# Performance work log

Measured on AMD Instinct MI355X. Metric: run time of the kernel, lower is better.

Reference implementation:

```python
import jax, jax.numpy as jnp
import numpy as np

B, D, G = 64, 1024, 64  # batch, features==units (required by the source einsum), num_groups


def setup_inputs() -> dict:
    key = jax.random.key(0)
    ks = jax.random.split(key, 8)
    return {
        "x": jax.random.normal(ks[0], (B, D), jnp.float32),
        "gid": jax.random.randint(ks[1], (B,), 0, G, dtype=jnp.int32),
        # mean-field variational parameters per group (weights flattened to D*D as in the source)
        "w_mu": jax.random.normal(ks[2], (G, D * D), jnp.float32) * 0.05,
        "w_sigma": jax.random.normal(ks[3], (G, D * D), jnp.float32) * 0.1 - 3.0,  # raw scale params
        "b_mu": jnp.zeros((G, D), jnp.float32),
        "b_sigma": jax.random.normal(ks[4], (G, D), jnp.float32) * 0.1 - 3.0,
        # reparameterization noise (explicit so forward is deterministic)
        "eps_w": jax.random.normal(ks[5], (B, D * D), jnp.float32),
        "eps_b": jax.random.normal(ks[6], (B, D), jnp.float32),
    }


def reference(x, gid, w_mu, w_sigma, b_mu, b_sigma, eps_w, eps_b):
    # Gather group-specific posterior params and sample via reparameterization.
    # scale = softplus(raw) matches the standard tfp mean-field parameterization.
    w_samp = w_mu[gid] + jax.nn.softplus(w_sigma[gid]) * eps_w  # (B, D*D)
    b_samp = b_mu[gid] + jax.nn.softplus(b_sigma[gid]) * eps_b  # (B, D)
    # Reshape((-1, units)): (B, num_features, units) = (B, D, D)
    w = w_samp.reshape(B, D, D)
    # tf.einsum('Bup,Bp->Bu', w, x): per-sample matmul (axis1 labeled u, axis2 labeled p)
    out = jnp.einsum("bup,bp->bu", w, x) + b_samp  # (B, D)
    return jax.nn.relu(out)
```

## Files before the change

kernel.cpp:

```cpp
#include <hip/hip_runtime.h>
#include <math.h>

#define BB 64
#define DD 1024
#define GG 64
#define F4 (DD / 4)
#define ROWS 2
#define WAVES_PB 4
#define U_PER_BLOCK (ROWS * WAVES_PB)
#define BLOCKS_PER_B (DD / U_PER_BLOCK)
#define NWG (BB * BLOCKS_PER_B)

typedef float fvec4 __attribute__((ext_vector_type(4)));

__device__ __forceinline__ float softplus_fast(float z) {
    const float LOG2E = 1.44269504088896340736f;
    const float LN2   = 0.69314718055994530942f;
    float t = __builtin_amdgcn_exp2f(-LOG2E * fabsf(z));
    float l = __builtin_amdgcn_logf(1.0f + t);
    return fmaxf(z, 0.0f) + LN2 * l;
}

__global__ __launch_bounds__(256) void mld_kernel(
    const float* __restrict__ x, const int* __restrict__ gid,
    const float* __restrict__ w_mu, const float* __restrict__ w_sigma,
    const float* __restrict__ b_mu, const float* __restrict__ b_sigma,
    const float* __restrict__ eps_w, const float* __restrict__ eps_b,
    float* __restrict__ out)
{
    const int lane = (int)(threadIdx.x & 63);
    const int wid  = (int)(threadIdx.x >> 6);

    const int logical = (int)blockIdx.x;
    const int b    = logical >> 7;
    const int ublk = logical & 127;
    const int u0   = ublk * U_PER_BLOCK + wid * ROWS;
    const int g    = gid[b];

    const fvec4* __restrict__ xr  = (const fvec4*)(x + (size_t)b * DD);
    const fvec4* __restrict__ wmr = (const fvec4*)(w_mu    + ((size_t)g * DD + u0) * DD);
    const fvec4* __restrict__ wsr = (const fvec4*)(w_sigma + ((size_t)g * DD + u0) * DD);
    const fvec4* __restrict__ ewr = (const fvec4*)(eps_w   + ((size_t)b * DD + u0) * DD);

    fvec4 X[4], WM0[4], WS0[4], EW0[4], WM1[4], WS1[4], EW1[4];
    #pragma unroll
    for (int k = 0; k < 4; ++k) {
        const int i = lane + 64 * k;
        X[k]   = xr[i];
        WM0[k] = wmr[i];
        WS0[k] = wsr[i];
        EW0[k] = __builtin_nontemporal_load(ewr + i);
        WM1[k] = wmr[F4 + i];
        WS1[k] = wsr[F4 + i];
        EW1[k] = __builtin_nontemporal_load(ewr + F4 + i);
    }
    asm volatile("" ::
        "v"(X[0]),   "v"(X[1]),   "v"(X[2]),   "v"(X[3]),
        "v"(WM0[0]), "v"(WM0[1]), "v"(WM0[2]), "v"(WM0[3]),
        "v"(WS0[0]), "v"(WS0[1]), "v"(WS0[2]), "v"(WS0[3]),
        "v"(EW0[0]), "v"(EW0[1]), "v"(EW0[2]), "v"(EW0[3]),
        "v"(WM1[0]), "v"(WM1[1]), "v"(WM1[2]), "v"(WM1[3]),
        "v"(WS1[0]), "v"(WS1[1]), "v"(WS1[2]), "v"(WS1[3]),
        "v"(EW1[0]), "v"(EW1[1]), "v"(EW1[2]), "v"(EW1[3]));

    float a0 = 0.f, a1 = 0.f;
    #pragma unroll
    for (int k = 0; k < 4; ++k) {
        a0 += (WM0[k].x + softplus_fast(WS0[k].x) * EW0[k].x) * X[k].x;
        a0 += (WM0[k].y + softplus_fast(WS0[k].y) * EW0[k].y) * X[k].y;
        a0 += (WM0[k].z + softplus_fast(WS0[k].z) * EW0[k].z) * X[k].z;
        a0 += (WM0[k].w + softplus_fast(WS0[k].w) * EW0[k].w) * X[k].w;
        a1 += (WM1[k].x + softplus_fast(WS1[k].x) * EW1[k].x) * X[k].x;
        a1 += (WM1[k].y + softplus_fast(WS1[k].y) * EW1[k].y) * X[k].y;
        a1 += (WM1[k].z + softplus_fast(WS1[k].z) * EW1[k].z) * X[k].z;
        a1 += (WM1[k].w + softplus_fast(WS1[k].w) * EW1[k].w) * X[k].w;
    }

    #pragma unroll
    for (int off = 32; off > 0; off >>= 1) {
        a0 += __shfl_xor(a0, off, 64);
        a1 += __shfl_xor(a1, off, 64);
    }

    if (lane < ROWS) {
        const int u = u0 + lane;
        const size_t gu = (size_t)g * DD + u;
        const size_t bu = (size_t)b * DD + u;
        const float eb = __builtin_nontemporal_load(eps_b + bu);
        const float bs = b_mu[gu] + softplus_fast(b_sigma[gu]) * eb;
        const float o = (lane == 0 ? a0 : a1) + bs;
        out[bu] = fmaxf(o, 0.0f);
    }
}

extern "C" void kernel_launch(void* const* d_in, const int* in_sizes, int n_in,
                              void* d_out, int out_size, void* d_ws, size_t ws_size,
                              hipStream_t stream) {
    const float* x       = (const float*)d_in[0];
    const int*   gid     = (const int*)d_in[1];
    const float* w_mu    = (const float*)d_in[2];
    const float* w_sigma = (const float*)d_in[3];
    const float* b_mu    = (const float*)d_in[4];
    const float* b_sigma = (const float*)d_in[5];
    const float* eps_w   = (const float*)d_in[6];
    const float* eps_b   = (const float*)d_in[7];
    float* out = (float*)d_out;

    mld_kernel<<<NWG, 256, 0, stream>>>(x, gid, w_mu, w_sigma, b_mu, b_sigma,
                                        eps_w, eps_b, out);
}
```

Before: 113.0 us.

## Group batch rows by gid so each group's weights and softplus are loaded once

Adds a small kernel that builds per-group lists of batch indices, then launches one grid over groups instead of batch rows. Each block loads w_mu and w_sigma for its group once, computes softplus once, and loops over every batch row in that group, streaming only eps_w and x per row. This removes the duplicated reads of the group weights and the repeated softplus when several rows share a group. The cost is an extra serial launch, load imbalance because row counts per group vary, and a loop that streams eps_w without the explicit register prefetch of the old code.

```diff
diff --git a/kernel.cpp b/kernel.cpp
--- a/kernel.cpp
+++ b/kernel.cpp
@@ -5,11 +5,9 @@
 #define DD 1024
 #define GG 64
 #define F4 (DD / 4)
-#define ROWS 2
-#define WAVES_PB 4
-#define U_PER_BLOCK (ROWS * WAVES_PB)
-#define BLOCKS_PER_B (DD / U_PER_BLOCK)
-#define NWG (BB * BLOCKS_PER_B)
+#define UPB 8
+#define BLOCKS_PER_G (DD / UPB)
+#define NWG (GG * BLOCKS_PER_G)
 
 typedef float fvec4 __attribute__((ext_vector_type(4)));
 
@@ -21,8 +19,20 @@
     return fmaxf(z, 0.0f) + LN2 * l;
 }
 
-__global__ __launch_bounds__(256) void mld_kernel(
-    const float* __restrict__ x, const int* __restrict__ gid,
+__global__ void build_lists(const int* __restrict__ gid,
+                            int* __restrict__ counts, int* __restrict__ lists) {
+    const int g = (int)threadIdx.x;
+    if (g < GG) {
+        int c = 0;
+        for (int b = 0; b < BB; ++b)
+            if (gid[b] == g) lists[g * BB + (c++)] = b;
+        counts[g] = c;
+    }
+}
+
+__global__ __launch_bounds__(256) void mld_group_kernel(
+    const float* __restrict__ x,
+    const int* __restrict__ counts, const int* __restrict__ lists,
     const float* __restrict__ w_mu, const float* __restrict__ w_sigma,
     const float* __restrict__ b_mu, const float* __restrict__ b_sigma,
     const float* __restrict__ eps_w, const float* __restrict__ eps_b,
@@ -30,66 +40,66 @@
 {
     const int lane = (int)(threadIdx.x & 63);
     const int wid  = (int)(threadIdx.x >> 6);
+    const int g    = (int)blockIdx.x >> 7;
+    const int ublk = (int)blockIdx.x & 127;
+    const int n    = counts[g];
+    if (n == 0) return;
+    const int u0   = ublk * UPB + wid * 2;
 
-    const int logical = (int)blockIdx.x;
-    const int b    = logical >> 7;
-    const int ublk = logical & 127;
-    const int u0   = ublk * U_PER_BLOCK + wid * ROWS;
-    const int g    = gid[b];
-
-    const fvec4* __restrict__ xr  = (const fvec4*)(x + (size_t)b * DD);
     const fvec4* __restrict__ wmr = (const fvec4*)(w_mu    + ((size_t)g * DD + u0) * DD);
     const fvec4* __restrict__ wsr = (const fvec4*)(w_sigma + ((size_t)g * DD + u0) * DD);
-    const fvec4* __restrict__ ewr = (const fvec4*)(eps_w   + ((size_t)b * DD + u0) * DD);
 
-    fvec4 X[4], WM0[4], WS0[4], EW0[4], WM1[4], WS1[4], EW1[4];
+    fvec4 WM0[4], WM1[4], SP0[4], SP1[4];
     #pragma unroll
     for (int k = 0; k < 4; ++k) {
         const int i = lane + 64 * k;
-        X[k]   = xr[i];
         WM0[k] = wmr[i];
-        WS0[k] = wsr[i];
-        EW0[k] = __builtin_nontemporal_load(ewr + i);
         WM1[k] = wmr[F4 + i];
-        WS1[k] = wsr[F4 + i];
-        EW1[k] = __builtin_nontemporal_load(ewr + F4 + i);
-    }
-    asm volatile("" ::
-        "v"(X[0]),   "v"(X[1]),   "v"(X[2]),   "v"(X[3]),
-        "v"(WM0[0]), "v"(WM0[1]), "v"(WM0[2]), "v"(WM0[3]),
-        "v"(WS0[0]), "v"(WS0[1]), "v"(WS0[2]), "v"(WS0[3]),
-        "v"(EW0[0]), "v"(EW0[1]), "v"(EW0[2]), "v"(EW0[3]),
-        "v"(WM1[0]), "v"(WM1[1]), "v"(WM1[2]), "v"(WM1[3]),
-        "v"(WS1[0]), "v"(WS1[1]), "v"(WS1[2]), "v"(WS1[3]),
-        "v"(EW1[0]), "v"(EW1[1]), "v"(EW1[2]), "v"(EW1[3]));
-
-    float a0 = 0.f, a1 = 0.f;
-    #pragma unroll
-    for (int k = 0; k < 4; ++k) {
-        a0 += (WM0[k].x + softplus_fast(WS0[k].x) * EW0[k].x) * X[k].x;
-        a0 += (WM0[k].y + softplus_fast(WS0[k].y) * EW0[k].y) * X[k].y;
-        a0 += (WM0[k].z + softplus_fast(WS0[k].z) * EW0[k].z) * X[k].z;
-        a0 += (WM0[k].w + softplus_fast(WS0[k].w) * EW0[k].w) * X[k].w;
-        a1 += (WM1[k].x + softplus_fast(WS1[k].x) * EW1[k].x) * X[k].x;
-        a1 += (WM1[k].y + softplus_fast(WS1[k].y) * EW1[k].y) * X[k].y;
-        a1 += (WM1[k].z + softplus_fast(WS1[k].z) * EW1[k].z) * X[k].z;
-        a1 += (WM1[k].w + softplus_fast(WS1[k].w) * EW1[k].w) * X[k].w;
+        fvec4 s0 = wsr[i];
+        fvec4 s1 = wsr[F4 + i];
+        SP0[k].x = softplus_fast(s0.x); SP0[k].y = softplus_fast(s0.y);
+        SP0[k].z = softplus_fast(s0.z); SP0[k].w = softplus_fast(s0.w);
+        SP1[k].x = softplus_fast(s1.x); SP1[k].y = softplus_fast(s1.y);
+        SP1[k].z = softplus_fast(s1.z); SP1[k].w = softplus_fast(s1.w);
     }
 
-    #pragma unroll
-    for (int off = 32; off > 0; off >>= 1) {
-        a0 += __shfl_xor(a0, off, 64);
-        a1 += __shfl_xor(a1, off, 64);
-    }
+    for (int s = 0; s < n; ++s) {
+        const int b = lists[g * BB + s];
+        const fvec4* __restrict__ xr  = (const fvec4*)(x     + (size_t)b * DD);
+        const fvec4* __restrict__ ewr = (const fvec4*)(eps_w + ((size_t)b * DD + u0) * DD);
 
-    if (lane < ROWS) {
-        const int u = u0 + lane;
-        const size_t gu = (size_t)g * DD + u;
-        const size_t bu = (size_t)b * DD + u;
-        const float eb = __builtin_nontemporal_load(eps_b + bu);
-        const float bs = b_mu[gu] + softplus_fast(b_sigma[gu]) * eb;
-        const float o = (lane == 0 ? a0 : a1) + bs;
-        out[bu] = fmaxf(o, 0.0f);
+        float a0 = 0.f, a1 = 0.f;
+        #pragma unroll
+        for (int k = 0; k < 4; ++k) {
+            const int i = lane + 64 * k;
+            const fvec4 xm = xr[i];
+            const fvec4 e0 = __builtin_nontemporal_load(ewr + i);
+            const fvec4 e1 = __builtin_nontemporal_load(ewr + F4 + i);
+            a0 += (WM0[k].x + SP0[k].x * e0.x) * xm.x;
+            a0 += (WM0[k].y + SP0[k].y * e0.y) * xm.y;
+            a0 += (WM0[k].z + SP0[k].z * e0.z) * xm.z;
+            a0 += (WM0[k].w + SP0[k].w * e0.w) * xm.w;
+            a1 += (WM1[k].x + SP1[k].x * e1.x) * xm.x;
+            a1 += (WM1[k].y + SP1[k].y * e1.y) * xm.y;
+            a1 += (WM1[k].z + SP1[k].z * e1.z) * xm.z;
+            a1 += (WM1[k].w + SP1[k].w * e1.w) * xm.w;
+        }
+
+        #pragma unroll
+        for (int off = 32; off > 0; off >>= 1) {
+            a0 += __shfl_xor(a0, off, 64);
+            a1 += __shfl_xor(a1, off, 64);
+        }
+
+        if (lane < 2) {
+            const int u = u0 + lane;
+            const size_t gu = (size_t)g * DD + u;
+            const size_t bu = (size_t)b * DD + u;
+            const float eb = __builtin_nontemporal_load(eps_b + bu);
+            const float bs = b_mu[gu] + softplus_fast(b_sigma[gu]) * eb;
+            const float o = (lane == 0 ? a0 : a1) + bs;
+            out[bu] = fmaxf(o, 0.0f);
+        }
     }
 }
 
@@ -106,6 +116,10 @@
     const float* eps_b   = (const float*)d_in[7];
     float* out = (float*)d_out;
 
-    mld_kernel<<<NWG, 256, 0, stream>>>(x, gid, w_mu, w_sigma, b_mu, b_sigma,
-                                        eps_w, eps_b, out);
+    int* counts = (int*)d_ws;
+    int* lists  = counts + GG;
+
+    build_lists<<<1, 64, 0, stream>>>(gid, counts, lists);
+    mld_group_kernel<<<NWG, 256, 0, stream>>>(x, counts, lists, w_mu, w_sigma,
+                                              b_mu, b_sigma, eps_w, eps_b, out);
 }
```

Result: faster. 99.45 us (-12.0%).

## Sort batch rows by group so blocks sharing weights launch adjacently

Applied to the files above, without the earlier changes.

A small pre-kernel counting-sorts batch indices by group id into the workspace. The main kernel then maps block slots to samples in sorted order, so samples in the same group run close together and can reuse the cached w_mu/w_sigma rows. The explicit register staging with the asm barrier is also replaced by an interleaved load-compute loop. In exchange this adds an extra kernel launch and a serial scan, and the loads may be less batched.

```diff
diff --git a/kernel.cpp b/kernel.cpp
--- a/kernel.cpp
+++ b/kernel.cpp
@@ -6,9 +6,8 @@
 #define GG 64
 #define F4 (DD / 4)
 #define ROWS 2
-#define WAVES_PB 4
-#define U_PER_BLOCK (ROWS * WAVES_PB)
-#define BLOCKS_PER_B (DD / U_PER_BLOCK)
+#define UPB 8
+#define BLOCKS_PER_B (DD / UPB)
 #define NWG (BB * BLOCKS_PER_B)
 
 typedef float fvec4 __attribute__((ext_vector_type(4)));
@@ -21,8 +20,24 @@
     return fmaxf(z, 0.0f) + LN2 * l;
 }
 
+__global__ void build_sorted(const int* __restrict__ gid, int* __restrict__ sorted) {
+    const int g = (int)threadIdx.x;
+    int cnt = 0;
+    for (int b = 0; b < BB; ++b) cnt += (gid[b] == g) ? 1 : 0;
+    int pre = cnt;
+    #pragma unroll
+    for (int d = 1; d < 64; d <<= 1) {
+        int t = __shfl_up(pre, d, 64);
+        if (g >= d) pre += t;
+    }
+    int off = pre - cnt;
+    for (int b = 0; b < BB; ++b)
+        if (gid[b] == g) sorted[off++] = b;
+}
+
 __global__ __launch_bounds__(256) void mld_kernel(
     const float* __restrict__ x, const int* __restrict__ gid,
+    const int* __restrict__ sorted,
     const float* __restrict__ w_mu, const float* __restrict__ w_sigma,
     const float* __restrict__ b_mu, const float* __restrict__ b_sigma,
     const float* __restrict__ eps_w, const float* __restrict__ eps_b,
@@ -30,50 +45,36 @@
 {
     const int lane = (int)(threadIdx.x & 63);
     const int wid  = (int)(threadIdx.x >> 6);
-
-    const int logical = (int)blockIdx.x;
-    const int b    = logical >> 7;
-    const int ublk = logical & 127;
-    const int u0   = ublk * U_PER_BLOCK + wid * ROWS;
+    const int slot = (int)blockIdx.x >> 7;
+    const int ublk = (int)blockIdx.x & 127;
+    const int b    = sorted[slot];
     const int g    = gid[b];
+    const int u0   = ublk * UPB + wid * ROWS;
 
     const fvec4* __restrict__ xr  = (const fvec4*)(x + (size_t)b * DD);
     const fvec4* __restrict__ wmr = (const fvec4*)(w_mu    + ((size_t)g * DD + u0) * DD);
     const fvec4* __restrict__ wsr = (const fvec4*)(w_sigma + ((size_t)g * DD + u0) * DD);
     const fvec4* __restrict__ ewr = (const fvec4*)(eps_w   + ((size_t)b * DD + u0) * DD);
 
-    fvec4 X[4], WM0[4], WS0[4], EW0[4], WM1[4], WS1[4], EW1[4];
+    float a0 = 0.f, a1 = 0.f;
     #pragma unroll
     for (int k = 0; k < 4; ++k) {
         const int i = lane + 64 * k;
-        X[k]   = xr[i];
-        WM0[k] = wmr[i];
-        WS0[k] = wsr[i];
-        EW0[k] = __builtin_nontemporal_load(ewr + i);
-        WM1[k] = wmr[F4 + i];
-        WS1[k] = wsr[F4 + i];
-        EW1[k] = __builtin_nontemporal_load(ewr + F4 + i);
-    }
-    asm volatile("" ::
-        "v"(X[0]),   "v"(X[1]),   "v"(X[2]),   "v"(X[3]),
-        "v"(WM0[0]), "v"(WM0[1]), "v"(WM0[2]), "v"(WM0[3]),
-        "v"(WS0[0]), "v"(WS0[1]), "v"(WS0[2]), "v"(WS0[3]),
-        "v"(EW0[0]), "v"(EW0[1]), "v"(EW0[2]), "v"(EW0[3]),
-        "v"(WM1[0]), "v"(WM1[1]), "v"(WM1[2]), "v"(WM1[3]),
-        "v"(WS1[0]), "v"(WS1[1]), "v"(WS1[2]), "v"(WS1[3]),
-        "v"(EW1[0]), "v"(EW1[1]), "v"(EW1[2]), "v"(EW1[3]));
-
-    float a0 = 0.f, a1 = 0.f;
-    #pragma unroll
-    for (int k = 0; k < 4; ++k) {
-        a0 += (WM0[k].x + softplus_fast(WS0[k].x) * EW0[k].x) * X[k].x;
-        a0 += (WM0[k].y + softplus_fast(WS0[k].y) * EW0[k].y) * X[k].y;
-        a0 += (WM0[k].z + softplus_fast(WS0[k].z) * EW0[k].z) * X[k].z;
-        a0 += (WM0[k].w + softplus_fast(WS0[k].w) * EW0[k].w) * X[k].w;
-        a1 += (WM1[k].x + softplus_fast(WS1[k].x) * EW1[k].x) * X[k].x;
-        a1 += (WM1[k].y + softplus_fast(WS1[k].y) * EW1[k].y) * X[k].y;
-        a1 += (WM1[k].z + softplus_fast(WS1[k].z) * EW1[k].z) * X[k].z;
-        a1 += (WM1[k].w + softplus_fast(WS1[k].w) * EW1[k].w) * X[k].w;
+        const fvec4 xm = xr[i];
+        const fvec4 wm0 = wmr[i];
+        const fvec4 ws0 = wsr[i];
+        const fvec4 e0  = __builtin_nontemporal_load(ewr + i);
+        const fvec4 wm1 = wmr[F4 + i];
+        const fvec4 ws1 = wsr[F4 + i];
+        const fvec4 e1  = __builtin_nontemporal_load(ewr + F4 + i);
+        a0 += (wm0.x + softplus_fast(ws0.x) * e0.x) * xm.x;
+        a0 += (wm0.y + softplus_fast(ws0.y) * e0.y) * xm.y;
+        a0 += (wm0.z + softplus_fast(ws0.z) * e0.z) * xm.z;
+        a0 += (wm0.w + softplus_fast(ws0.w) * e0.w) * xm.w;
+        a1 += (wm1.x + softplus_fast(ws1.x) * e1.x) * xm.x;
+        a1 += (wm1.y + softplus_fast(ws1.y) * e1.y) * xm.y;
+        a1 += (wm1.z + softplus_fast(ws1.z) * e1.z) * xm.z;
+        a1 += (wm1.w + softplus_fast(ws1.w) * e1.w) * xm.w;
     }
 
     #pragma unroll
@@ -106,6 +107,9 @@
     const float* eps_b   = (const float*)d_in[7];
     float* out = (float*)d_out;
 
-    mld_kernel<<<NWG, 256, 0, stream>>>(x, gid, w_mu, w_sigma, b_mu, b_sigma,
-                                        eps_w, eps_b, out);
+    int* sorted = (int*)d_ws;
+
+    build_sorted<<<1, 64, 0, stream>>>(gid, sorted);
+    mld_kernel<<<NWG, 256, 0, stream>>>(x, gid, sorted, w_mu, w_sigma,
+                                        b_mu, b_sigma, eps_w, eps_b, out);
 }
```

New measurement: 98.84 us. 12.5% less time.
